# Optimization experiments

Hardware: AMD Instinct MI355X
Metric: run time of the kernel (lower is better)

## Reference

```python
import jax, jax.numpy as jnp
import numpy as np

NUM_CLASSES = 512  # static number of distinct labels (all present in targets)
EPS = 1e-8         # torch.nn.CosineSimilarity default eps


def setup_inputs() -> dict:
    N, D, C = 65536, 256, NUM_CLASSES
    key = jax.random.key(0)
    k1, k2 = jax.random.split(key)
    inputs = jax.random.normal(k1, (N, D), dtype=jnp.float32)
    # every label 0..C-1 appears -> sorted-unique remap in the torch code is identity
    targets = jax.random.permutation(k2, jnp.arange(N, dtype=jnp.int32) % C)
    return {"inputs": inputs, "targets": targets}


def reference(inputs, targets):
    C = NUM_CLASSES
    # per-label segment mean (prototypes), replacing the python unique/mask loop
    sums = jax.ops.segment_sum(inputs, targets, num_segments=C)          # [C, D]
    counts = jax.ops.segment_sum(jnp.ones((inputs.shape[0],), inputs.dtype),
                                 targets, num_segments=C)                # [C]
    protos = sums / counts[:, None]                                       # [C, D]

    # pairwise cosine similarity: x.p / max(|x||p|, eps)
    dots = inputs @ protos.T                                              # [N, C]
    n_in = jnp.linalg.norm(inputs, axis=-1)                               # [N]
    n_pr = jnp.linalg.norm(protos, axis=-1)                               # [C]
    sim = dots / jnp.maximum(n_in[:, None] * n_pr[None, :], EPS)          # [N, C]

    # cross entropy, mean reduction (labels already equal mapped targets)
    logp = jax.nn.log_softmax(sim, axis=-1)                               # [N, C]
    nll = -jnp.take_along_axis(logp, targets[:, None].astype(jnp.int32), axis=-1)[:, 0]
    return jnp.mean(nll)
```

## Files before the change

### kernel.cpp

```cpp
#include <hip/hip_runtime.h>
#include <math.h>

#define NROWS 65536
#define DIM   256
#define NCLS  512
#define CPW   128
#define BMAIN 256
#define NSUB  4
#define NBLK  (NROWS / BMAIN)

#define WS_CNT_I   0
#define WS_IDX_I   512
#define WS_QPACK_F 66048

typedef float f32x4  __attribute__((ext_vector_type(4)));
typedef short bf16x8 __attribute__((ext_vector_type(8)));
typedef unsigned short u16;

__device__ inline u16 f2bf(float f) {
  unsigned u = __float_as_uint(f);
  u += 0x7FFFu + ((u >> 16) & 1u);
  return (u16)(u >> 16);
}
__device__ inline unsigned pack2(float a, float b) {
  return (unsigned)f2bf(a) | ((unsigned)f2bf(b) << 16);
}

__global__ __launch_bounds__(512) void k_zero(int* __restrict__ cnt,
                                              float* __restrict__ out) {
  cnt[threadIdx.x] = 0;
  if (threadIdx.x == 0) out[0] = 0.f;
}

__global__ __launch_bounds__(256) void k_scatter(
    const int* __restrict__ tgt, int* __restrict__ cnt, int* __restrict__ idx) {
  const int row = blockIdx.x * 256 + threadIdx.x;
  const int c = tgt[row];
  const int p = atomicAdd(&cnt[c], 1);
  if (p < CPW) idx[c * CPW + p] = row;
}

__global__ __launch_bounds__(512) void k_csum(
    const float* __restrict__ x, const int* __restrict__ idx,
    u16* __restrict__ qpack) {
  __shared__ int   sidx[CPW];
  __shared__ float wpart[8][DIM];
  __shared__ float wsum[4];
  __shared__ float ninv_s;
  const int c    = blockIdx.x;
  const int tid  = threadIdx.x;
  const int w    = tid >> 6;
  const int lane = tid & 63;
  if (tid < CPW) sidx[tid] = idx[c * CPW + tid];
  __syncthreads();

  float4 a4[4];
  #pragma unroll
  for (int j = 0; j < 4; ++j) a4[j] = make_float4(0.f, 0.f, 0.f, 0.f);
  #pragma unroll
  for (int i = 0; i < 4; ++i) {
    #pragma unroll
    for (int j = 0; j < 4; ++j) {
      const int row = sidx[w * 16 + i * 4 + j];
      const float4 v = *reinterpret_cast<const float4*>(
          x + (size_t)row * DIM + lane * 4);
      a4[j].x += v.x; a4[j].y += v.y; a4[j].z += v.z; a4[j].w += v.w;
    }
  }
  float4 vs;
  vs.x = (a4[0].x + a4[1].x) + (a4[2].x + a4[3].x);
  vs.y = (a4[0].y + a4[1].y) + (a4[2].y + a4[3].y);
  vs.z = (a4[0].z + a4[1].z) + (a4[2].z + a4[3].z);
  vs.w = (a4[0].w + a4[1].w) + (a4[2].w + a4[3].w);
  *reinterpret_cast<float4*>(&wpart[w][lane * 4]) = vs;
  __syncthreads();

  float s = 0.f;
  if (tid < DIM) {
    #pragma unroll
    for (int ww = 0; ww < 8; ++ww) s += wpart[ww][tid];
  }
  float sq = s * s;
  sq += __shfl_xor(sq, 1, 64);
  sq += __shfl_xor(sq, 2, 64);
  sq += __shfl_xor(sq, 4, 64);
  sq += __shfl_xor(sq, 8, 64);
  sq += __shfl_xor(sq, 16, 64);
  sq += __shfl_xor(sq, 32, 64);
  if (tid < DIM && (tid & 63) == 0) wsum[tid >> 6] = sq;
  __syncthreads();
  if (tid == 0) ninv_s = rsqrtf(fmaxf(wsum[0] + wsum[1] + wsum[2] + wsum[3], 1e-30f));
  __syncthreads();
  if (tid < DIM)
    qpack[((tid >> 3) * NCLS + c) * 8 + (tid & 7)] = f2bf(s * ninv_s);
}

__global__ __launch_bounds__(512, 2) void k_main(
    const float* __restrict__ x, const int* __restrict__ tgt,
    const u16* __restrict__ qpack, float* __restrict__ out) {
  __shared__ u16   Alds[32 * 64 * 8] __attribute__((aligned(16)));
  __shared__ float psum[8][64];
  __shared__ float simt[64];
  __shared__ int   ltgt[64];

  const int tid  = threadIdx.x;
  const int w    = tid >> 6;
  const int lane = tid & 63;
  const int lg   = lane >> 4, l15 = lane & 15;
  const int row  = tid >> 3;
  const int part = tid & 7;

  const bf16x8* bp = reinterpret_cast<const bf16x8*>(qpack);
  const int bbase = w * 64 + l15;
  bf16x8 B[8][4];
  #pragma unroll
  for (int kk = 0; kk < 8; ++kk)
    #pragma unroll
    for (int n = 0; n < 4; ++n)
      B[kk][n] = bp[(kk * 4 + lg) * NCLS + bbase + n * 16];

  float block_loss = 0.f;

  #pragma unroll 1
  for (int s = 0; s < NSUB; ++s) {
    const int r0 = blockIdx.x * BMAIN + s * 64;

    {
      const float4* xr = reinterpret_cast<const float4*>(
          x + (size_t)(r0 + row) * DIM + part * 32);
      float4 v[8];
      #pragma unroll
      for (int j = 0; j < 8; ++j) v[j] = xr[j];
      float ss = 0.f;
      #pragma unroll
      for (int j = 0; j < 8; ++j)
        ss += v[j].x * v[j].x + v[j].y * v[j].y + v[j].z * v[j].z + v[j].w * v[j].w;
      ss += __shfl_xor(ss, 1, 64);
      ss += __shfl_xor(ss, 2, 64);
      ss += __shfl_xor(ss, 4, 64);
      const float rn = rsqrtf(fmaxf(ss, 1e-30f));
      #pragma unroll
      for (int jj = 0; jj < 4; ++jj) {
        uint4 wv;
        wv.x = pack2(v[2*jj].x * rn,   v[2*jj].y * rn);
        wv.y = pack2(v[2*jj].z * rn,   v[2*jj].w * rn);
        wv.z = pack2(v[2*jj+1].x * rn, v[2*jj+1].y * rn);
        wv.w = pack2(v[2*jj+1].z * rn, v[2*jj+1].w * rn);
        const int kg = part * 4 + jj;
        const int rs = row ^ part;
        *reinterpret_cast<uint4*>(&Alds[(kg * 64 + rs) * 8]) = wv;
      }
    }
    if (tid < 64) ltgt[tid] = tgt[r0 + tid];
    __syncthreads();

    f32x4 acc[4][4];
    #pragma unroll
    for (int m = 0; m < 4; ++m)
      #pragma unroll
      for (int n = 0; n < 4; ++n) acc[m][n] = (f32x4)0.f;

    #pragma unroll
    for (int kk = 0; kk < 8; ++kk) {
      bf16x8 a[4];
      #pragma unroll
      for (int m = 0; m < 4; ++m)
        a[m] = *reinterpret_cast<const bf16x8*>(
            &Alds[((kk * 4 + lg) * 64 + ((m * 16 + l15) ^ kk)) * 8]);
      #pragma unroll
      for (int m = 0; m < 4; ++m)
        #pragma unroll
        for (int n = 0; n < 4; ++n)
          acc[m][n] = __builtin_amdgcn_mfma_f32_16x16x32_bf16(a[m], B[kk][n], acc[m][n], 0, 0, 0);
    }

    #pragma unroll
    for (int m = 0; m < 4; ++m) {
      #pragma unroll
      for (int reg = 0; reg < 4; ++reg) {
        const int r = m * 16 + lg * 4 + reg;
        float sx = __expf(acc[m][0][reg]) + __expf(acc[m][1][reg]) +
                   __expf(acc[m][2][reg]) + __expf(acc[m][3][reg]);
        sx += __shfl_xor(sx, 1, 64);
        sx += __shfl_xor(sx, 2, 64);
        sx += __shfl_xor(sx, 4, 64);
        sx += __shfl_xor(sx, 8, 64);
        if (l15 == 0) psum[w][r] = sx;
        const int tg = ltgt[r];
        if (w == (tg >> 6) && l15 == (tg & 15)) {
          const int nt = (tg >> 4) & 3;
          float pv = acc[m][0][reg];
          pv = (nt == 1) ? acc[m][1][reg] : pv;
          pv = (nt == 2) ? acc[m][2][reg] : pv;
          pv = (nt == 3) ? acc[m][3][reg] : pv;
          simt[r] = pv;
        }
      }
    }
    __syncthreads();
    if (tid < 64) {
      float sum = 0.f;
      #pragma unroll
      for (int ww = 0; ww < 8; ++ww) sum += psum[ww][tid];
      float lr = __logf(sum) - simt[tid];
      lr += __shfl_xor(lr, 1, 64);
      lr += __shfl_xor(lr, 2, 64);
      lr += __shfl_xor(lr, 4, 64);
      lr += __shfl_xor(lr, 8, 64);
      lr += __shfl_xor(lr, 16, 64);
      lr += __shfl_xor(lr, 32, 64);
      block_loss += lr;
    }
  }
  if (tid == 0) atomicAdd(out, block_loss * (1.0f / (float)NROWS));
}

extern "C" void kernel_launch(void* const* d_in, const int* in_sizes, int n_in,
                              void* d_out, int out_size, void* d_ws, size_t ws_size,
                              hipStream_t stream) {
  const float* x   = (const float*)d_in[0];
  const int*   tgt = (const int*)d_in[1];
  float* ws    = (float*)d_ws;
  int*   cnt   = (int*)ws + WS_CNT_I;
  int*   idx   = (int*)ws + WS_IDX_I;
  u16*   qpack = (u16*)(ws + WS_QPACK_F);
  float* out   = (float*)d_out;

  k_zero<<<1, 512, 0, stream>>>(cnt, out);
  k_scatter<<<NROWS / 256, 256, 0, stream>>>(tgt, cnt, idx);
  k_csum<<<NCLS, 512, 0, stream>>>(x, idx, qpack);
  k_main<<<NBLK, 512, 0, stream>>>(x, tgt, qpack, out);
}
```

Baseline: 84.64 us.

## Stream prototype tiles from global and prefetch next row tile during MFMA

```diff
diff --git a/kernel.cpp b/kernel.cpp
--- a/kernel.cpp
+++ b/kernel.cpp
@@ -1,12 +1,13 @@
 #include <hip/hip_runtime.h>
+#include <hip/hip_bf16.h>
 #include <math.h>
 
 #define NROWS 65536
 #define DIM   256
 #define NCLS  512
 #define CPW   128
-#define BMAIN 256
-#define NSUB  4
+#define NSUB  2
+#define BMAIN (64 * NSUB)
 #define NBLK  (NROWS / BMAIN)
 
 #define WS_CNT_I   0
@@ -23,7 +24,8 @@
   return (u16)(u >> 16);
 }
 __device__ inline unsigned pack2(float a, float b) {
-  return (unsigned)f2bf(a) | ((unsigned)f2bf(b) << 16);
+  __hip_bfloat162 h = __float22bfloat162_rn(make_float2(a, b));
+  return *reinterpret_cast<unsigned*>(&h);
 }
 
 __global__ __launch_bounds__(512) void k_zero(int* __restrict__ cnt,
@@ -95,13 +97,36 @@
     qpack[((tid >> 3) * NCLS + c) * 8 + (tid & 7)] = f2bf(s * ninv_s);
 }
 
-__global__ __launch_bounds__(512, 2) void k_main(
+__device__ inline void normpack(const float4 v[8], u16* __restrict__ dst,
+                                int row, int part) {
+  float ss = 0.f;
+  #pragma unroll
+  for (int j = 0; j < 8; ++j)
+    ss += v[j].x * v[j].x + v[j].y * v[j].y + v[j].z * v[j].z + v[j].w * v[j].w;
+  ss += __shfl_xor(ss, 1, 64);
+  ss += __shfl_xor(ss, 2, 64);
+  ss += __shfl_xor(ss, 4, 64);
+  const float rn = rsqrtf(fmaxf(ss, 1e-30f));
+  #pragma unroll
+  for (int jj = 0; jj < 4; ++jj) {
+    uint4 wv;
+    wv.x = pack2(v[2*jj].x * rn,   v[2*jj].y * rn);
+    wv.y = pack2(v[2*jj].z * rn,   v[2*jj].w * rn);
+    wv.z = pack2(v[2*jj+1].x * rn, v[2*jj+1].y * rn);
+    wv.w = pack2(v[2*jj+1].z * rn, v[2*jj+1].w * rn);
+    const int kg = part * 4 + jj;
+    const int rs = row ^ part;
+    *reinterpret_cast<uint4*>(&dst[(kg * 64 + rs) * 8]) = wv;
+  }
+}
+
+__global__ __launch_bounds__(512, 4) void k_main(
     const float* __restrict__ x, const int* __restrict__ tgt,
     const u16* __restrict__ qpack, float* __restrict__ out) {
-  __shared__ u16   Alds[32 * 64 * 8] __attribute__((aligned(16)));
+  __shared__ u16   Alds[NSUB][32 * 64 * 8] __attribute__((aligned(16)));
   __shared__ float psum[8][64];
   __shared__ float simt[64];
-  __shared__ int   ltgt[64];
+  __shared__ int   ltgt[BMAIN];
 
   const int tid  = threadIdx.x;
   const int w    = tid >> 6;
@@ -109,69 +134,61 @@
   const int lg   = lane >> 4, l15 = lane & 15;
   const int row  = tid >> 3;
   const int part = tid & 7;
+  const size_t rbase = (size_t)blockIdx.x * BMAIN;
 
   const bf16x8* bp = reinterpret_cast<const bf16x8*>(qpack);
   const int bbase = w * 64 + l15;
-  bf16x8 B[8][4];
-  #pragma unroll
-  for (int kk = 0; kk < 8; ++kk)
-    #pragma unroll
-    for (int n = 0; n < 4; ++n)
-      B[kk][n] = bp[(kk * 4 + lg) * NCLS + bbase + n * 16];
+
+  float4 v[8];
+  {
+    const float4* xr = reinterpret_cast<const float4*>(
+        x + (rbase + row) * DIM + part * 32);
+    #pragma unroll
+    for (int j = 0; j < 8; ++j) v[j] = xr[j];
+  }
+  if (tid < BMAIN) ltgt[tid] = tgt[rbase + tid];
+  normpack(v, &Alds[0][0], row, part);
+  __syncthreads();
 
   float block_loss = 0.f;
 
-  #pragma unroll 1
+  #pragma unroll
   for (int s = 0; s < NSUB; ++s) {
-    const int r0 = blockIdx.x * BMAIN + s * 64;
-
-    {
+    if (s + 1 < NSUB) {
       const float4* xr = reinterpret_cast<const float4*>(
-          x + (size_t)(r0 + row) * DIM + part * 32);
-      float4 v[8];
+          x + (rbase + (s + 1) * 64 + row) * DIM + part * 32);
       #pragma unroll
       for (int j = 0; j < 8; ++j) v[j] = xr[j];
-      float ss = 0.f;
-      #pragma unroll
-      for (int j = 0; j < 8; ++j)
-        ss += v[j].x * v[j].x + v[j].y * v[j].y + v[j].z * v[j].z + v[j].w * v[j].w;
-      ss += __shfl_xor(ss, 1, 64);
-      ss += __shfl_xor(ss, 2, 64);
-      ss += __shfl_xor(ss, 4, 64);
-      const float rn = rsqrtf(fmaxf(ss, 1e-30f));
-      #pragma unroll
-      for (int jj = 0; jj < 4; ++jj) {
-        uint4 wv;
-        wv.x = pack2(v[2*jj].x * rn,   v[2*jj].y * rn);
-        wv.y = pack2(v[2*jj].z * rn,   v[2*jj].w * rn);
-        wv.z = pack2(v[2*jj+1].x * rn, v[2*jj+1].y * rn);
-        wv.w = pack2(v[2*jj+1].z * rn, v[2*jj+1].w * rn);
-        const int kg = part * 4 + jj;
-        const int rs = row ^ part;
-        *reinterpret_cast<uint4*>(&Alds[(kg * 64 + rs) * 8]) = wv;
+    }
+
+    f32x4 acc[4][4];
+    #pragma unroll
+    for (int m = 0; m < 4; ++m)
+      #pragma unroll
+      for (int n = 0; n < 4; ++n) acc[m][n] = (f32x4)0.f;
+
+    const u16* al = &Alds[s][0];
+    #pragma unroll 1
+    for (int kk = 0; kk < 8; ++kk) {
+      const int arow = (lg + kk * 4) * 64;
+      bf16x8 b0 = bp[(kk * 4 + lg) * NCLS + bbase];
+      bf16x8 b1 = bp[(kk * 4 + lg) * NCLS + bbase + 16];
+      #pragma unroll
+      for (int m = 0; m < 4; ++m) {
+        const bf16x8 a = *reinterpret_cast<const bf16x8*>(
+            &al[(arow + ((m * 16 + l15) ^ kk)) * 8]);
+        acc[m][0] = __builtin_amdgcn_mfma_f32_16x16x32_bf16(a, b0, acc[m][0], 0, 0, 0);
+        acc[m][1] = __builtin_amdgcn_mfma_f32_16x16x32_bf16(a, b1, acc[m][1], 0, 0, 0);
       }
-    }
-    if (tid < 64) ltgt[tid] = tgt[r0 + tid];
-    __syncthreads();
-
-    f32x4 acc[4][4];
-    #pragma unroll
-    for (int m = 0; m < 4; ++m)
-      #pragma unroll
-      for (int n = 0; n < 4; ++n) acc[m][n] = (f32x4)0.f;
-
-    #pragma unroll
-    for (int kk = 0; kk < 8; ++kk) {
-      bf16x8 a[4];
-      #pragma unroll
-      for (int m = 0; m < 4; ++m)
-        a[m] = *reinterpret_cast<const bf16x8*>(
-            &Alds[((kk * 4 + lg) * 64 + ((m * 16 + l15) ^ kk)) * 8]);
-      #pragma unroll
-      for (int m = 0; m < 4; ++m)
-        #pragma unroll
-        for (int n = 0; n < 4; ++n)
-          acc[m][n] = __builtin_amdgcn_mfma_f32_16x16x32_bf16(a[m], B[kk][n], acc[m][n], 0, 0, 0);
+      bf16x8 b2 = bp[(kk * 4 + lg) * NCLS + bbase + 32];
+      bf16x8 b3 = bp[(kk * 4 + lg) * NCLS + bbase + 48];
+      #pragma unroll
+      for (int m = 0; m < 4; ++m) {
+        const bf16x8 a = *reinterpret_cast<const bf16x8*>(
+            &al[(arow + ((m * 16 + l15) ^ kk)) * 8]);
+        acc[m][2] = __builtin_amdgcn_mfma_f32_16x16x32_bf16(a, b2, acc[m][2], 0, 0, 0);
+        acc[m][3] = __builtin_amdgcn_mfma_f32_16x16x32_bf16(a, b3, acc[m][3], 0, 0, 0);
+      }
     }
 
     #pragma unroll
@@ -186,7 +203,7 @@
         sx += __shfl_xor(sx, 4, 64);
         sx += __shfl_xor(sx, 8, 64);
         if (l15 == 0) psum[w][r] = sx;
-        const int tg = ltgt[r];
+        const int tg = ltgt[s * 64 + r];
         if (w == (tg >> 6) && l15 == (tg & 15)) {
           const int nt = (tg >> 4) & 3;
           float pv = acc[m][0][reg];
@@ -210,6 +227,10 @@
       lr += __shfl_xor(lr, 16, 64);
       lr += __shfl_xor(lr, 32, 64);
       block_loss += lr;
+    }
+    if (s + 1 < NSUB) {
+      normpack(v, &Alds[s + 1][0], row, part);
+      __syncthreads();
     }
   }
   if (tid == 0) atomicAdd(out, block_loss * (1.0f / (float)NROWS));
```

Result: faster. 82.63 us (median of 4 runs) (-2.4%).
